# Optimization experiments

Hardware: AMD Instinct MI355X
Metric: run time of the kernel (lower is better)

The kernel has to match this reference:

```python
import jax, jax.numpy as jnp
import numpy as np

EPS = 1e-5
B, CIN, L = 512, 5, 1024   # batch, input channels, msp length == d_model
COUT, A, NB = 32, 13, 5    # CNN branch channels, max_atoms, num_bonds_prediction


def conv1d(x, w, pad, groups=1):
    # x: (N, C, L), w: (O, I/groups, K)
    return jax.lax.conv_general_dilated(
        x, w, window_strides=(1,), padding=[(pad, pad)],
        dimension_numbers=("NCH", "OIH", "NCH"), feature_group_count=groups)


def batchnorm(x, g, b):
    # training-mode BN over (N, L) per channel, as nn.BatchNorm1d in train()
    m = jnp.mean(x, axis=(0, 2), keepdims=True)
    v = jnp.var(x, axis=(0, 2), keepdims=True)
    return (x - m) * jax.lax.rsqrt(v + EPS) * g[None, :, None] + b[None, :, None]


def setup_inputs() -> dict:
    key = jax.random.key(0)
    ks = jax.random.split(key, 16)
    n = jax.random.normal
    inp = {
        "src": n(ks[0], (B, CIN, L), dtype=jnp.float32),
        "mask": jnp.ones((B, A), dtype=bool),
        "max_atoms": A,
        # CNN branch 1 (kernel 5) : depthwise, pointwise, BN, residual 1x1 conv
        "dw1": n(ks[1], (CIN, 1, 5), dtype=jnp.float32) * 0.2,
        "pw1": n(ks[2], (COUT, CIN, 1), dtype=jnp.float32) * 0.2,
        "g1": jnp.ones((COUT,), jnp.float32),
        "be1": jnp.zeros((COUT,), jnp.float32),
        "r1w": n(ks[3], (COUT, CIN, 1), dtype=jnp.float32) * 0.2,
        "r1b": jnp.zeros((COUT,), jnp.float32),
        # CNN branch 2 (kernel 3)
        "dw2": n(ks[4], (CIN, 1, 3), dtype=jnp.float32) * 0.2,
        "pw2": n(ks[5], (COUT, CIN, 1), dtype=jnp.float32) * 0.2,
        "g2": jnp.ones((COUT,), jnp.float32),
        "be2": jnp.zeros((COUT,), jnp.float32),
        "r2w": n(ks[6], (COUT, CIN, 1), dtype=jnp.float32) * 0.2,
        "r2b": jnp.zeros((COUT,), jnp.float32),
        # EdgeClassify2 linears: ll1 (2*COUT -> A), fl (2*L -> NB)
        "ll1w": n(ks[7], (A, 2 * COUT), dtype=jnp.float32) * 0.1,
        "ll1b": jnp.zeros((A,), jnp.float32),
        "flw": n(ks[8], (NB, 2 * L), dtype=jnp.float32) * 0.02,
        "flb": jnp.zeros((NB,), jnp.float32),
    }
    return inp


def reference(src, mask, max_atoms, dw1, pw1, g1, be1, r1w, r1b,
              dw2, pw2, g2, be2, r2w, r2b, ll1w, ll1b, flw, flb):
    # ---- CNN encoder ----
    e1 = jax.nn.relu(batchnorm(conv1d(conv1d(src, dw1, 2, groups=CIN), pw1, 0), g1, be1))
    e1 = e1 * (conv1d(src, r1w, 0) + r1b[None, :, None])
    e2 = jax.nn.relu(batchnorm(conv1d(conv1d(src, dw2, 1, groups=CIN), pw2, 0), g2, be2))
    e2 = e2 * (conv1d(src, r2w, 0) + r2b[None, :, None])
    x = jnp.concatenate([e1, e2], axis=1)          # (B, 2*COUT, L)
    # ---- EdgeClassify2 ----
    # ll1 over channel dim: (B, 2*COUT, L) -> (B, A, L)
    h = jnp.einsum("bcl,ac->bal", x, ll1w) + ll1b[None, :, None]
    # vectorized replacement of the O(A^2) python loop:
    # final_e[:, i, j] = concat(h[:, min(i,j)], h[:, max(i,j)])
    idx = jnp.arange(max_atoms)
    mn = jnp.minimum(idx[:, None], idx[None, :])   # (A, A)
    mx = jnp.maximum(idx[:, None], idx[None, :])
    final_e = jnp.concatenate([h[:, mn, :], h[:, mx, :]], axis=-1)  # (B, A, A, 2L)
    out = jnp.einsum("bijd,nd->bijn", final_e, flw) + flb           # (B, A, A, NB)
    return out
```

## Files before the change

### kernel.cpp

```cpp
#include <hip/hip_runtime.h>
#include <hip/hip_bf16.h>

#define BB 512
#define LL 1024
#define AA 13
#define NBP 5
#define NTOT (BB * LL)
#define EPSV 1e-5f

#define WS_F     192
#define WS_PART  256
#define WS_CONST 10496

template<int CTRL, int RM, bool BC>
__device__ __forceinline__ float dppadd(float v) {
    int t = __builtin_amdgcn_update_dpp(0, __float_as_int(v), CTRL, RM, 0xf, BC);
    return v + __int_as_float(t);
}
__device__ __forceinline__ float wave_sum(float v) {
    v = dppadd<0x111, 0xf, true >(v);
    v = dppadd<0x112, 0xf, true >(v);
    v = dppadd<0x114, 0xf, true >(v);
    v = dppadd<0x118, 0xf, true >(v);
    v = dppadd<0x142, 0xa, false>(v);
    v = dppadd<0x143, 0xc, false>(v);
    return v;
}

__global__ __launch_bounds__(256) void k_moments(
    const float* __restrict__ src,
    const float* __restrict__ dw1,
    const float* __restrict__ dw2,
    const float* __restrict__ flw,
    float* __restrict__ ws)
{
    __shared__ float red[4][40];
    __shared__ float fred[4];
    int tid = threadIdx.x;
    int gid = blockIdx.x * 256 + tid;
    int b = gid >> 7, L0 = (gid & 127) << 3;
    const float* sb = src + b * (5 * LL);

    float w1[5][5], w2[5][3];
#pragma unroll
    for (int c = 0; c < 5; c++) {
#pragma unroll
        for (int t = 0; t < 5; t++) w1[c][t] = dw1[c*5+t];
#pragma unroll
        for (int t = 0; t < 3; t++) w2[c][t] = dw2[c*3+t];
    }

    float x[5][16];
#pragma unroll
    for (int c5 = 0; c5 < 5; c5++) {
        const float* sp = sb + c5 * LL;
        float4 xa = (L0 >= 4)    ? *(const float4*)(sp + L0 - 4) : make_float4(0,0,0,0);
        float4 xb = *(const float4*)(sp + L0);
        float4 xc = *(const float4*)(sp + L0 + 4);
        float4 xd = (L0 <= 1012) ? *(const float4*)(sp + L0 + 8) : make_float4(0,0,0,0);
        x[c5][0]=xa.x; x[c5][1]=xa.y; x[c5][2]=xa.z; x[c5][3]=xa.w;
        x[c5][4]=xb.x; x[c5][5]=xb.y; x[c5][6]=xb.z; x[c5][7]=xb.w;
        x[c5][8]=xc.x; x[c5][9]=xc.y; x[c5][10]=xc.z; x[c5][11]=xc.w;
        x[c5][12]=xd.x; x[c5][13]=xd.y; x[c5][14]=xd.z; x[c5][15]=xd.w;
    }

    float acc[40];
#pragma unroll
    for (int k = 0; k < 40; k++) acc[k] = 0.f;

#pragma unroll
    for (int k = 0; k < 8; k++) {
        float d1[5], d2[5];
#pragma unroll
        for (int c5 = 0; c5 < 5; c5++) {
            d1[c5] = w1[c5][0]*x[c5][k+2] + w1[c5][1]*x[c5][k+3] + w1[c5][2]*x[c5][k+4]
                   + w1[c5][3]*x[c5][k+5] + w1[c5][4]*x[c5][k+6];
            d2[c5] = w2[c5][0]*x[c5][k+3] + w2[c5][1]*x[c5][k+4] + w2[c5][2]*x[c5][k+5];
        }
#pragma unroll
        for (int j = 0; j < 5; j++) { acc[j] += d1[j]; acc[20+j] += d2[j]; }
#pragma unroll
        for (int j = 0; j < 5; j++)
#pragma unroll
            for (int kk = j; kk < 5; kk++) {
                int idx = j*(11-j)/2 + (kk - j);
                acc[5+idx]  += d1[j]*d1[kk];
                acc[25+idx] += d2[j]*d2[kk];
            }
    }

    int lane = tid & 63, wv = tid >> 6;
#pragma unroll
    for (int k = 0; k < 40; k++) acc[k] = wave_sum(acc[k]);
    if (lane == 63) {
#pragma unroll
        for (int k = 0; k < 40; k++) red[wv][k] = acc[k];
    }
    __syncthreads();
    if (tid < 40) {
        ws[WS_PART + blockIdx.x * 40 + tid] =
            red[0][tid] + red[1][tid] + red[2][tid] + red[3][tid];
    }

    if (blockIdx.x < 10) {
        int nn = blockIdx.x;
        int n = nn < 5 ? nn : nn - 5;
        int off = nn < 5 ? 0 : LL;
        float4 v = *(const float4*)(flw + n * (2*LL) + off + tid * 4);
        float s = wave_sum(v.x + v.y + v.z + v.w);
        if (lane == 63) fred[wv] = s;
        __syncthreads();
        if (tid == 0) ws[WS_F + nn] = fred[0] + fred[1] + fred[2] + fred[3];
    }
}

__global__ __launch_bounds__(320) void k_prep(
    float* __restrict__ ws,
    const float* __restrict__ pw1, const float* __restrict__ pw2,
    const float* __restrict__ g1,  const float* __restrict__ be1,
    const float* __restrict__ g2,  const float* __restrict__ be2,
    const float* __restrict__ r1w, const float* __restrict__ r2w,
    const float* __restrict__ r1b, const float* __restrict__ r2b)
{
    __shared__ float momS[40];
    int tid = threadIdx.x;
    {
        int k = tid >> 3, sub = tid & 7;
        float v = 0.f;
#pragma unroll 8
        for (int t2 = 0; t2 < 32; t2++) v += ws[WS_PART + (sub + (t2 << 3)) * 40 + k];
        v += __shfl_xor(v, 1, 64);
        v += __shfl_xor(v, 2, 64);
        v += __shfl_xor(v, 4, 64);
        if (sub == 0) momS[k] = v;
    }
    __syncthreads();
    if (tid < 64) {
        int brc = tid >> 5, o = tid & 31;
        const float invN = 1.0f / (float)NTOT;
        const float* pw = brc ? pw2 : pw1;
        const float* rw = brc ? r2w : r1w;
        const float* s  = momS + (brc ? 20 : 0);
        const float* M  = momS + (brc ? 25 : 5);
        float pwv[5], rwv[5], md[5];
#pragma unroll
        for (int j = 0; j < 5; j++) { pwv[j] = pw[o*5+j]; rwv[j] = rw[o*5+j]; md[j] = s[j] * invN; }
        float meanY = 0.f;
#pragma unroll
        for (int j = 0; j < 5; j++) meanY += pwv[j] * md[j];
        float ey2 = 0.f;
#pragma unroll
        for (int j = 0; j < 5; j++)
#pragma unroll
            for (int k = 0; k < 5; k++) {
                int lo = j < k ? j : k, hi = j < k ? k : j;
                int idx = lo*(11-lo)/2 + (hi - lo);
                ey2 += pwv[j] * pwv[k] * (M[idx] * invN);
            }
        float varY = ey2 - meanY * meanY;
        if (varY < 0.f) varY = 0.f;
        float gg = brc ? g2[o] : g1[o];
        float bb = brc ? be2[o] : be1[o];
        float rb = brc ? r2b[o] : r1b[o];
        float sc = gg * rsqrtf(varY + EPSV);
        float sh = bb - meanY * sc;
        float* dst = ws + WS_CONST + tid * 16;
        dst[0] = pwv[0]*sc; dst[1] = pwv[1]*sc; dst[2] = pwv[2]*sc; dst[3] = pwv[3]*sc;
        dst[4] = pwv[4]*sc; dst[5] = sh;        dst[6] = rb;        dst[7] = 0.f;
        dst[8] = rwv[0];    dst[9] = rwv[1];    dst[10] = rwv[2];   dst[11] = rwv[3];
        dst[12] = rwv[4];   dst[13] = 0.f;      dst[14] = 0.f;      dst[15] = 0.f;
    }
}

__global__ __launch_bounds__(512, 2) void k_fused(
    const float* __restrict__ src,
    const float* __restrict__ dw1,
    const float* __restrict__ dw2,
    const float* __restrict__ flw,
    const float* __restrict__ ll1w,
    const float* __restrict__ ll1b,
    const float* __restrict__ flb,
    const float* __restrict__ ws,
    float* __restrict__ out)
{
    __shared__ __align__(16) float srcS[5][1040];
    __shared__ __align__(16) float SLds[64][12];
    __shared__ float llT[832];
    __shared__ float PQ[130];

    int tid = threadIdx.x, b = blockIdx.x;
    int lane = tid & 63;
    int gu = __builtin_amdgcn_readfirstlane(tid >> 6);
    int br = gu >> 2;

    const float* srcB = src + b * (5 * LL);

    for (int idx = tid; idx < 5 * 256; idx += 512) {
        int c5 = idx >> 8, q = idx & 255;
        float4 v = *(const float4*)(srcB + (c5 << 10) + (q << 2));
        *(float4*)&srcS[c5][(q << 2) + 8] = v;
    }
    if (tid < 40) {
        int c5 = tid >> 3, j = tid & 7;
        int i = (j < 4) ? (4 + j) : (1028 + j);
        srcS[c5][i] = 0.f;
    }
    for (int idx = tid; idx < 832; idx += 512) {
        int cc = idx / 13, a = idx - cc * 13;
        llT[idx] = ll1w[a * 64 + cc];
    }
    __syncthreads();

    float wdw[5][5];
    if (br == 0) {
#pragma unroll
        for (int c5 = 0; c5 < 5; c5++)
#pragma unroll
            for (int t = 0; t < 5; t++) wdw[c5][t] = dw1[c5*5+t];
    } else {
#pragma unroll
        for (int c5 = 0; c5 < 5; c5++) {
            wdw[c5][0] = 0.f;
            wdw[c5][1] = dw2[c5*3+0]; wdw[c5][2] = dw2[c5*3+1]; wdw[c5][3] = dw2[c5*3+2];
            wdw[c5][4] = 0.f;
        }
    }
    const float* cb = ws + WS_CONST + (gu << 7);

    float acc[80];
#pragma unroll
    for (int k = 0; k < 80; k++) acc[k] = 0.f;
    int c0 = gu << 3;

#pragma unroll 1
    for (int p = 0; p < 4; p++) {
        int l0 = (p << 8) + (lane << 2);
        float fwv[10][4];
#pragma unroll
        for (int nn = 0; nn < 10; nn++) {
            int n = nn < 5 ? nn : nn - 5;
            int off = nn < 5 ? 0 : LL;
            float4 t4 = *(const float4*)(flw + n * (2*LL) + off + l0);
            fwv[nn][0] = t4.x; fwv[nn][1] = t4.y; fwv[nn][2] = t4.z; fwv[nn][3] = t4.w;
        }
        float dv[5][4], sv[5][4];
#pragma unroll
        for (int c5 = 0; c5 < 5; c5++) {
            int i0 = l0 + 8;
            float4 xa = *(const float4*)&srcS[c5][i0 - 4];
            float4 xb = *(const float4*)&srcS[c5][i0];
            float4 xc = *(const float4*)&srcS[c5][i0 + 4];
            float xx[12] = {xa.x, xa.y, xa.z, xa.w, xb.x, xb.y, xb.z, xb.w, xc.x, xc.y, xc.z, xc.w};
            sv[c5][0] = xb.x; sv[c5][1] = xb.y; sv[c5][2] = xb.z; sv[c5][3] = xb.w;
            if (br == 0) {
#pragma unroll
                for (int q = 0; q < 4; q++)
                    dv[c5][q] = wdw[c5][0]*xx[q+2] + wdw[c5][1]*xx[q+3] + wdw[c5][2]*xx[q+4]
                              + wdw[c5][3]*xx[q+5] + wdw[c5][4]*xx[q+6];
            } else {
#pragma unroll
                for (int q = 0; q < 4; q++)
                    dv[c5][q] = wdw[c5][1]*xx[q+3] + wdw[c5][2]*xx[q+4] + wdw[c5][3]*xx[q+5];
            }
        }
#pragma unroll
        for (int ci = 0; ci < 8; ci++) {
            const float4 A  = *(const float4*)(cb + ci*16);
            const float4 B2 = *(const float4*)(cb + ci*16 + 4);
            const float4 R0 = *(const float4*)(cb + ci*16 + 8);
            const float4 R1 = *(const float4*)(cb + ci*16 + 12);
            float e[4];
#pragma unroll
            for (int q = 0; q < 4; q++) {
                float y = B2.y + A.x*dv[0][q] + A.y*dv[1][q] + A.z*dv[2][q]
                                + A.w*dv[3][q] + B2.x*dv[4][q];
                float r = B2.z + R0.x*sv[0][q] + R0.y*sv[1][q] + R0.z*sv[2][q]
                                + R0.w*sv[3][q] + R1.x*sv[4][q];
                e[q] = fmaxf(y, 0.f) * r;
            }
#pragma unroll
            for (int nn = 0; nn < 10; nn++) {
                acc[ci*10 + nn] += e[0]*fwv[nn][0] + e[1]*fwv[nn][1]
                                 + e[2]*fwv[nn][2] + e[3]*fwv[nn][3];
            }
        }
    }

#pragma unroll
    for (int k = 0; k < 80; k++) acc[k] = wave_sum(acc[k]);
    if (lane == 63) {
#pragma unroll
        for (int ci = 0; ci < 8; ci++) {
            int c = c0 + ci;
            *(float4*)&SLds[c][0] = make_float4(acc[ci*10+0], acc[ci*10+1], acc[ci*10+2], acc[ci*10+3]);
            *(float4*)&SLds[c][4] = make_float4(acc[ci*10+4], acc[ci*10+5], acc[ci*10+6], acc[ci*10+7]);
            *(float2*)&SLds[c][8] = make_float2(acc[ci*10+8], acc[ci*10+9]);
        }
    }
    __syncthreads();

    if (tid < 130) {
        int half = tid >= 65 ? 1 : 0;
        int q = tid - half * 65;
        int a = q / 5, n = q - a * 5;
        int col = half * 5 + n;
        float v = ll1b[a] * ws[WS_F + col];
#pragma unroll 8
        for (int cc = 0; cc < 64; cc++) v += llT[cc * 13 + a] * SLds[cc][col];
        PQ[tid] = v;
    }
    __syncthreads();

    for (int idx = tid; idx < AA * AA * NBP; idx += 512) {
        int i = idx / 65;
        int rr = idx - i * 65;
        int j = rr / 5, n = rr - j * 5;
        int mn = i < j ? i : j, mx = i < j ? j : i;
        out[b * (AA * AA * NBP) + idx] = PQ[mn * 5 + n] + PQ[65 + mx * 5 + n] + flb[n];
    }
}

extern "C" void kernel_launch(void* const* d_in, const int* in_sizes, int n_in,
                              void* d_out, int out_size, void* d_ws, size_t ws_size,
                              hipStream_t stream) {
    const float* src  = (const float*)d_in[0];
    const float* dw1  = (const float*)d_in[3];
    const float* pw1  = (const float*)d_in[4];
    const float* g1   = (const float*)d_in[5];
    const float* be1  = (const float*)d_in[6];
    const float* r1w  = (const float*)d_in[7];
    const float* r1b  = (const float*)d_in[8];
    const float* dw2  = (const float*)d_in[9];
    const float* pw2  = (const float*)d_in[10];
    const float* g2   = (const float*)d_in[11];
    const float* be2  = (const float*)d_in[12];
    const float* r2w  = (const float*)d_in[13];
    const float* r2b  = (const float*)d_in[14];
    const float* ll1w = (const float*)d_in[15];
    const float* ll1b = (const float*)d_in[16];
    const float* flw  = (const float*)d_in[17];
    const float* flb  = (const float*)d_in[18];
    float* ws  = (float*)d_ws;
    float* out = (float*)d_out;

    k_moments<<<256, 256, 0, stream>>>(src, dw1, dw2, flw, ws);
    k_prep<<<1, 320, 0, stream>>>(ws, pw1, pw2, g1, be1, g2, be2, r1w, r2w, r1b, r2b);
    k_fused<<<BB, 512, 0, stream>>>(src, dw1, dw2, flw, ll1w, ll1b, flb, ws, out);
}
```

Baseline: 152.7 us.

## Double block to 1024 threads, halve channels per wave, stage flw in LDS

The fused kernel now launches 1024 threads per block, so each wave handles 4 output channels instead of 8 and accumulator registers drop from 80 to 40. The final-linear weights flw are staged in shared memory in two halves instead of being re-read from global memory per pass, and the per-channel constants are hoisted into registers. This aims to raise occupancy and cut redundant global loads. The cost is extra block-wide barriers for the second flw half, recomputing the depthwise conv across twice as many waves, and a larger shared-memory footprint.

```diff
diff --git a/kernel.cpp b/kernel.cpp
--- a/kernel.cpp
+++ b/kernel.cpp
@@ -172,7 +172,7 @@
     }
 }
 
-__global__ __launch_bounds__(512, 2) void k_fused(
+__global__ __launch_bounds__(1024, 1) void k_fused(
     const float* __restrict__ src,
     const float* __restrict__ dw1,
     const float* __restrict__ dw2,
@@ -184,18 +184,20 @@
     float* __restrict__ out)
 {
     __shared__ __align__(16) float srcS[5][1040];
+    __shared__ __align__(16) float flwS[10][512];
     __shared__ __align__(16) float SLds[64][12];
     __shared__ float llT[832];
     __shared__ float PQ[130];
 
     int tid = threadIdx.x, b = blockIdx.x;
     int lane = tid & 63;
-    int gu = __builtin_amdgcn_readfirstlane(tid >> 6);
-    int br = gu >> 2;
+    int w = __builtin_amdgcn_readfirstlane(tid >> 6);
+    int br = w >> 3;
+    int c0 = w << 2;
 
     const float* srcB = src + b * (5 * LL);
 
-    for (int idx = tid; idx < 5 * 256; idx += 512) {
+    for (int idx = tid; idx < 5 * 256; idx += 1024) {
         int c5 = idx >> 8, q = idx & 255;
         float4 v = *(const float4*)(srcB + (c5 << 10) + (q << 2));
         *(float4*)&srcS[c5][(q << 2) + 8] = v;
@@ -205,92 +207,114 @@
         int i = (j < 4) ? (4 + j) : (1028 + j);
         srcS[c5][i] = 0.f;
     }
-    for (int idx = tid; idx < 832; idx += 512) {
-        int cc = idx / 13, a = idx - cc * 13;
-        llT[idx] = ll1w[a * 64 + cc];
-    }
-    __syncthreads();
-
-    float wdw[5][5];
+    if (tid < 832) {
+        int cc = tid / 13, a = tid - cc * 13;
+        llT[tid] = ll1w[a * 64 + cc];
+    }
+    for (int idx = tid; idx < 1280; idx += 1024) {
+        int nn = idx >> 7, q = idx & 127;
+        int n = nn < 5 ? nn : nn - 5;
+        int off = nn < 5 ? 0 : LL;
+        float4 v = *(const float4*)(flw + n * (2*LL) + off + (q << 2));
+        *(float4*)&flwS[nn][q << 2] = v;
+    }
+
+    float tap[5][5];
     if (br == 0) {
 #pragma unroll
         for (int c5 = 0; c5 < 5; c5++)
 #pragma unroll
-            for (int t = 0; t < 5; t++) wdw[c5][t] = dw1[c5*5+t];
+            for (int t = 0; t < 5; t++) tap[c5][t] = dw1[c5*5+t];
     } else {
 #pragma unroll
         for (int c5 = 0; c5 < 5; c5++) {
-            wdw[c5][0] = 0.f;
-            wdw[c5][1] = dw2[c5*3+0]; wdw[c5][2] = dw2[c5*3+1]; wdw[c5][3] = dw2[c5*3+2];
-            wdw[c5][4] = 0.f;
-        }
-    }
-    const float* cb = ws + WS_CONST + (gu << 7);
-
-    float acc[80];
-#pragma unroll
-    for (int k = 0; k < 80; k++) acc[k] = 0.f;
-    int c0 = gu << 3;
+#pragma unroll
+            for (int t = 0; t < 3; t++) tap[c5][t] = dw2[c5*3+t];
+            tap[c5][3] = 0.f; tap[c5][4] = 0.f;
+        }
+    }
+    const float* cb = ws + WS_CONST + (c0 << 4);
+    float Ac[4][5], Rc[4][5], shv[4], rbv[4];
+#pragma unroll
+    for (int ci = 0; ci < 4; ci++) {
+#pragma unroll
+        for (int j = 0; j < 5; j++) { Ac[ci][j] = cb[ci*16 + j]; Rc[ci][j] = cb[ci*16 + 8 + j]; }
+        shv[ci] = cb[ci*16 + 5];
+        rbv[ci] = cb[ci*16 + 6];
+    }
+
+    float acc[40];
+#pragma unroll
+    for (int k = 0; k < 40; k++) acc[k] = 0.f;
+
+    __syncthreads();
 
 #pragma unroll 1
-    for (int p = 0; p < 4; p++) {
-        int l0 = (p << 8) + (lane << 2);
-        float fwv[10][4];
-#pragma unroll
-        for (int nn = 0; nn < 10; nn++) {
-            int n = nn < 5 ? nn : nn - 5;
-            int off = nn < 5 ? 0 : LL;
-            float4 t4 = *(const float4*)(flw + n * (2*LL) + off + l0);
-            fwv[nn][0] = t4.x; fwv[nn][1] = t4.y; fwv[nn][2] = t4.z; fwv[nn][3] = t4.w;
-        }
-        float dv[5][4], sv[5][4];
-#pragma unroll
-        for (int c5 = 0; c5 < 5; c5++) {
-            int i0 = l0 + 8;
-            float4 xa = *(const float4*)&srcS[c5][i0 - 4];
-            float4 xb = *(const float4*)&srcS[c5][i0];
-            float4 xc = *(const float4*)&srcS[c5][i0 + 4];
-            float xx[12] = {xa.x, xa.y, xa.z, xa.w, xb.x, xb.y, xb.z, xb.w, xc.x, xc.y, xc.z, xc.w};
-            sv[c5][0] = xb.x; sv[c5][1] = xb.y; sv[c5][2] = xb.z; sv[c5][3] = xb.w;
-            if (br == 0) {
-#pragma unroll
-                for (int q = 0; q < 4; q++)
-                    dv[c5][q] = wdw[c5][0]*xx[q+2] + wdw[c5][1]*xx[q+3] + wdw[c5][2]*xx[q+4]
-                              + wdw[c5][3]*xx[q+5] + wdw[c5][4]*xx[q+6];
-            } else {
-#pragma unroll
-                for (int q = 0; q < 4; q++)
-                    dv[c5][q] = wdw[c5][1]*xx[q+3] + wdw[c5][2]*xx[q+4] + wdw[c5][3]*xx[q+5];
-            }
-        }
-#pragma unroll
-        for (int ci = 0; ci < 8; ci++) {
-            const float4 A  = *(const float4*)(cb + ci*16);
-            const float4 B2 = *(const float4*)(cb + ci*16 + 4);
-            const float4 R0 = *(const float4*)(cb + ci*16 + 8);
-            const float4 R1 = *(const float4*)(cb + ci*16 + 12);
-            float e[4];
-#pragma unroll
-            for (int q = 0; q < 4; q++) {
-                float y = B2.y + A.x*dv[0][q] + A.y*dv[1][q] + A.z*dv[2][q]
-                                + A.w*dv[3][q] + B2.x*dv[4][q];
-                float r = B2.z + R0.x*sv[0][q] + R0.y*sv[1][q] + R0.z*sv[2][q]
-                                + R0.w*sv[3][q] + R1.x*sv[4][q];
-                e[q] = fmaxf(y, 0.f) * r;
+    for (int h = 0; h < 2; h++) {
+        if (h == 1) {
+            __syncthreads();
+            for (int idx = tid; idx < 1280; idx += 1024) {
+                int nn = idx >> 7, q = idx & 127;
+                int n = nn < 5 ? nn : nn - 5;
+                int off = nn < 5 ? 0 : LL;
+                float4 v = *(const float4*)(flw + n * (2*LL) + off + 512 + (q << 2));
+                *(float4*)&flwS[nn][q << 2] = v;
+            }
+            __syncthreads();
+        }
+#pragma unroll
+        for (int ploc = 0; ploc < 2; ploc++) {
+            int lq = (ploc << 8) + (lane << 2);
+            int i0 = (h << 9) + lq + 8;
+            float dv[5][4], sv[5][4];
+#pragma unroll
+            for (int c5 = 0; c5 < 5; c5++) {
+                float4 xa = *(const float4*)&srcS[c5][i0 - 4];
+                float4 xb = *(const float4*)&srcS[c5][i0];
+                float4 xc = *(const float4*)&srcS[c5][i0 + 4];
+                float xx[12] = {xa.x, xa.y, xa.z, xa.w, xb.x, xb.y, xb.z, xb.w, xc.x, xc.y, xc.z, xc.w};
+                sv[c5][0] = xb.x; sv[c5][1] = xb.y; sv[c5][2] = xb.z; sv[c5][3] = xb.w;
+                if (br == 0) {
+#pragma unroll
+                    for (int q = 0; q < 4; q++)
+                        dv[c5][q] = tap[c5][0]*xx[q+2] + tap[c5][1]*xx[q+3] + tap[c5][2]*xx[q+4]
+                                  + tap[c5][3]*xx[q+5] + tap[c5][4]*xx[q+6];
+                } else {
+#pragma unroll
+                    for (int q = 0; q < 4; q++)
+                        dv[c5][q] = tap[c5][0]*xx[q+3] + tap[c5][1]*xx[q+4] + tap[c5][2]*xx[q+5];
+                }
+            }
+            float e[4][4];
+#pragma unroll
+            for (int ci = 0; ci < 4; ci++) {
+#pragma unroll
+                for (int q = 0; q < 4; q++) {
+                    float y = shv[ci], r = rbv[ci];
+#pragma unroll
+                    for (int j = 0; j < 5; j++) {
+                        y = fmaf(Ac[ci][j], dv[j][q], y);
+                        r = fmaf(Rc[ci][j], sv[j][q], r);
+                    }
+                    e[ci][q] = fmaxf(y, 0.f) * r;
+                }
             }
 #pragma unroll
             for (int nn = 0; nn < 10; nn++) {
-                acc[ci*10 + nn] += e[0]*fwv[nn][0] + e[1]*fwv[nn][1]
-                                 + e[2]*fwv[nn][2] + e[3]*fwv[nn][3];
-            }
-        }
-    }
-
-#pragma unroll
-    for (int k = 0; k < 80; k++) acc[k] = wave_sum(acc[k]);
+                float4 f4 = *(const float4*)&flwS[nn][lq];
+#pragma unroll
+                for (int ci = 0; ci < 4; ci++)
+                    acc[ci*10+nn] += e[ci][0]*f4.x + e[ci][1]*f4.y
+                                   + e[ci][2]*f4.z + e[ci][3]*f4.w;
+            }
+        }
+    }
+
+#pragma unroll
+    for (int k = 0; k < 40; k++) acc[k] = wave_sum(acc[k]);
     if (lane == 63) {
 #pragma unroll
-        for (int ci = 0; ci < 8; ci++) {
+        for (int ci = 0; ci < 4; ci++) {
             int c = c0 + ci;
             *(float4*)&SLds[c][0] = make_float4(acc[ci*10+0], acc[ci*10+1], acc[ci*10+2], acc[ci*10+3]);
             *(float4*)&SLds[c][4] = make_float4(acc[ci*10+4], acc[ci*10+5], acc[ci*10+6], acc[ci*10+7]);
@@ -311,12 +335,12 @@
     }
     __syncthreads();
 
-    for (int idx = tid; idx < AA * AA * NBP; idx += 512) {
-        int i = idx / 65;
-        int rr = idx - i * 65;
+    if (tid < AA * AA * NBP) {
+        int i = tid / 65;
+        int rr = tid - i * 65;
         int j = rr / 5, n = rr - j * 5;
         int mn = i < j ? i : j, mx = i < j ? j : i;
-        out[b * (AA * AA * NBP) + idx] = PQ[mn * 5 + n] + PQ[65 + mx * 5 + n] + flb[n];
+        out[b * (AA * AA * NBP) + tid] = PQ[mn * 5 + n] + PQ[65 + mx * 5 + n] + flb[n];
     }
 }
 
@@ -345,5 +369,5 @@
 
     k_moments<<<256, 256, 0, stream>>>(src, dw1, dw2, flw, ws);
     k_prep<<<1, 320, 0, stream>>>(ws, pw1, pw2, g1, be1, g2, be2, r1w, r2w, r1b, r2b);
-    k_fused<<<BB, 512, 0, stream>>>(src, dw1, dw2, flw, ll1w, ll1b, flb, ws, out);
-}
+    k_fused<<<BB, 1024, 0, stream>>>(src, dw1, dw2, flw, ll1w, ll1b, flb, ws, out);
+}
```

Result: slower. 207.1 us (+35.6%).
